# Optimization experiments

Measured on AMD Instinct MI355X. Metric: run time of the kernel, lower is better.

Reference implementation:

```python
import jax, jax.numpy as jnp
import numpy as np

B, T, D, U = 4096, 50, 128, 128  # batch, history len, embed dim, GRU units (U==D)
ATT_H1, ATT_H2 = 128, 64         # Attention MLP hiddens (hard-coded in source)
DH1, DH2 = 256, 128              # deep model hiddens
BN_EPS = 1e-3
LEAKY = 0.0003


def setup_inputs() -> dict:
    key = jax.random.key(0)
    ks = iter(jax.random.split(key, 40))
    n = lambda shape, s=0.05: jax.random.normal(next(ks), shape, dtype=jnp.float32) * s
    DI = U + D  # deep_input dim
    return {
        "inputs": n((B, T + 1, D), 1.0),
        # Keras GRU (reset_after=True): kernel, recurrent kernel, bias[2,3U] (input/recurrent)
        "gru_W": n((D, 3 * U)), "gru_U": n((U, 3 * U)), "gru_b": n((2, 3 * U)),
        # Attention MLP: input is concat([h, news-h, news, h*news]) -> 4U
        "att_W1": n((4 * U, ATT_H1)), "att_b1": n((ATT_H1,)),
        "att_W2": n((ATT_H1, ATT_H2)), "att_b2": n((ATT_H2,)),
        "att_W3": n((ATT_H2, 1)), "att_b3": n((1,)),
        # AUGRU Bilinear gates: Dense(U, bias) on inputs, Dense(U, no bias) on state
        "au_Wu": n((U, U)), "au_bu": n((U,)), "au_Uu": n((U, U)),
        "au_Wr": n((U, U)), "au_br": n((U,)), "au_Ur": n((U, U)),
        "au_Wc": n((U, U)), "au_bc": n((U,)), "au_Uc": n((U, U)),
        # deep model: BN (inference) + 2 leaky-relu Dense + sigmoid head
        "bn_gamma": jnp.ones((DI,), jnp.float32), "bn_beta": jnp.zeros((DI,), jnp.float32),
        "bn_mean": jnp.zeros((DI,), jnp.float32), "bn_var": jnp.ones((DI,), jnp.float32),
        "d_W1": n((DI, DH1)), "d_b1": n((DH1,)),
        "d_W2": n((DH1, DH2)), "d_b2": n((DH2,)),
        "f_W": n((DH2, 1)), "f_b": n((1,)),
    }


def _gru(x_seq, W, Ur, b):
    # Keras GRU, reset_after=True, gate order [z, r, h]
    Xp = jnp.einsum('btd,dk->btk', x_seq, W) + b[0]  # precompute input projections
    h0 = jnp.zeros((x_seq.shape[0], Ur.shape[0]), x_seq.dtype)

    def step(h, xp):
        hp = h @ Ur + b[1]
        xz, xr, xh = jnp.split(xp, 3, axis=-1)
        hz, hr, hh = jnp.split(hp, 3, axis=-1)
        z = jax.nn.sigmoid(xz + hz)
        r = jax.nn.sigmoid(xr + hr)
        hc = jnp.tanh(xh + r * hh)
        hn = z * h + (1.0 - z) * hc
        return hn, hn

    _, hs = jax.lax.scan(step, h0, jnp.swapaxes(Xp, 0, 1))
    return jnp.swapaxes(hs, 0, 1)  # [B,T,U]


def reference(inputs, gru_W, gru_U, gru_b,
              att_W1, att_b1, att_W2, att_b2, att_W3, att_b3,
              au_Wu, au_bu, au_Uu, au_Wr, au_br, au_Ur, au_Wc, au_bc, au_Uc,
              bn_gamma, bn_beta, bn_mean, bn_var,
              d_W1, d_b1, d_W2, d_b2, f_W, f_b):
    hist = inputs[:, :-1, :]   # [B,T,D]
    news = inputs[:, -1, :]    # [B,D]

    hs = _gru(hist, gru_W, gru_U, gru_b)  # [B,T,U]

    # Attention (vectorized over the per-timestep Python loop; same math)
    news_b = jnp.broadcast_to(news[:, None, :], hs.shape)
    emb = jnp.concatenate([hs, news_b - hs, news_b, hs * news_b], axis=-1)  # [B,T,4U]
    a = jax.nn.relu(jnp.einsum('bti,ij->btj', emb, att_W1) + att_b1)
    a = jax.nn.relu(jnp.einsum('bti,ij->btj', a, att_W2) + att_b2)
    ats = jax.nn.sigmoid(jnp.einsum('bti,ij->btj', a, att_W3) + att_b3)  # [B,T,1]

    # AUGRU: precompute input-side projections, scan the recurrence
    xu = jnp.einsum('btd,dk->btk', hs, au_Wu) + au_bu
    xr = jnp.einsum('btd,dk->btk', hs, au_Wr) + au_br
    xc = jnp.einsum('btd,dk->btk', hs, au_Wc) + au_bc

    def au_step(h, xs):
        xu_t, xr_t, xc_t, at_t = xs
        u = jax.nn.sigmoid(xu_t + h @ au_Uu)
        r = jax.nn.sigmoid(xr_t + h @ au_Ur)
        c = jnp.tanh(xc_t + r * (h @ au_Uc))
        u_ = at_t * u
        hn = (1.0 - u_) * h + u_ * c
        return hn, None

    h0 = jnp.zeros_like(hs[:, 0, :])
    xs = (jnp.swapaxes(xu, 0, 1), jnp.swapaxes(xr, 0, 1),
          jnp.swapaxes(xc, 0, 1), jnp.swapaxes(ats, 0, 1))
    h_final, _ = jax.lax.scan(au_step, h0, xs)

    # deep model: BN (inference) -> Dense + leaky ReLU x2 -> sigmoid head
    x = jnp.concatenate([h_final, news], axis=-1)
    x = (x - bn_mean) * jax.lax.rsqrt(bn_var + BN_EPS) * bn_gamma + bn_beta
    x = x @ d_W1 + d_b1
    x = jnp.where(x >= 0, x, LEAKY * x)
    x = x @ d_W2 + d_b2
    x = jnp.where(x >= 0, x, LEAKY * x)
    y = jax.nn.sigmoid(x @ f_W + f_b)  # [B,1]
    return y
```

## Files before the change

kernel.cpp:

```cpp
#include <hip/hip_runtime.h>
#include <hip/hip_bf16.h>
#include <math.h>


#define LK 0.0003f

typedef __attribute__((ext_vector_type(8))) short short8;
typedef __attribute__((ext_vector_type(4))) float f32x4;

union U8 { short8 s; unsigned short u[8]; };

__device__ __forceinline__ float sigf(float x) {
    return __builtin_amdgcn_rcpf(1.0f + __expf(-x));
}
__device__ __forceinline__ float tanhfast(float x) {
    return fmaf(2.0f, __builtin_amdgcn_rcpf(1.0f + __expf(-2.0f * x)), -1.0f);
}
__device__ __forceinline__ float lky(float v) { return v >= 0.0f ? v : LK * v; }
__device__ __forceinline__ unsigned short f2bf(float f) {
    __bf16 b = (__bf16)f;
    return *reinterpret_cast<unsigned short*>(&b);
}
__device__ __forceinline__ unsigned pk2(float a, float b) {
    return (unsigned)f2bf(a) | ((unsigned)f2bf(b) << 16);
}
__device__ __forceinline__ float bf2f(unsigned short h) {
    return __uint_as_float(((unsigned)h) << 16);
}
__device__ __forceinline__ int swz(int row, int kbyte, int stride) {
    return row * stride + (kbyte ^ ((row & 7) << 4));
}
__device__ __forceinline__ f32x4 mfma16(short8 a, short8 b, f32x4 c) {
    return __builtin_amdgcn_mfma_f32_16x16x32_bf16(a, b, c, 0, 0, 0);
}
__device__ __forceinline__ void barrier_lds() {
    __builtin_amdgcn_sched_barrier(0);
    asm volatile("s_waitcnt lgkmcnt(0)" ::: "memory");
    __builtin_amdgcn_sched_barrier(0);
    __builtin_amdgcn_s_barrier();
    __builtin_amdgcn_sched_barrier(0);
}

__global__ void pack_all(
    const float* __restrict__ gW, const float* __restrict__ gU,
    const float* __restrict__ aWu, const float* __restrict__ aWr, const float* __restrict__ aWc,
    const float* __restrict__ aUu, const float* __restrict__ aUr, const float* __restrict__ aUc,
    const float* __restrict__ tW1, const float* __restrict__ tW2,
    const float* __restrict__ dW1, const float* __restrict__ dW2,
    const float* __restrict__ abu, const float* __restrict__ abr, const float* __restrict__ abc,
    unsigned short* __restrict__ Wg, unsigned short* __restrict__ Ug,
    unsigned short* __restrict__ Wau, unsigned short* __restrict__ Uau,
    unsigned short* __restrict__ WA, unsigned short* __restrict__ WN,
    unsigned short* __restrict__ AW2,
    unsigned short* __restrict__ DW1, unsigned short* __restrict__ DW2,
    float* __restrict__ bp)
{
    int i = blockIdx.x * 256 + threadIdx.x;
    if (i < 49152) {
        int n = i >> 7, k = i & 127;
        Wg[i] = f2bf(gW[k * 384 + n]);
        Ug[i] = f2bf(gU[k * 384 + n]);
    } else if (i < 98304) {
        int j = i - 49152; int n = j >> 7, k = j & 127;
        int g = n >> 7, c = n & 127;
        const float* s = (g == 0) ? aWu : (g == 1) ? aWr : aWc;
        const float* u = (g == 0) ? aUu : (g == 1) ? aUr : aUc;
        Wau[j] = f2bf(s[k * 128 + c]);
        Uau[j] = f2bf(u[k * 128 + c]);
    } else if (i < 131072) {
        int j = i - 98304; int n = j >> 8, k = j & 255;
        float v = (k < 128) ? (tW1[k * 128 + n] - tW1[(128 + k) * 128 + n])
                            : tW1[(384 + (k - 128)) * 128 + n];
        WA[j] = f2bf(v);
    } else if (i < 147456) {
        int j = i - 131072; int n = j >> 7, k = j & 127;
        WN[j] = f2bf(tW1[(128 + k) * 128 + n] + tW1[(256 + k) * 128 + n]);
    } else if (i < 155648) {
        int j = i - 147456; int n = j >> 7, k = j & 127;
        AW2[j] = f2bf(tW2[k * 64 + n]);
    } else if (i < 221184) {
        int j = i - 155648; int n = j >> 8, k = j & 255;
        DW1[j] = f2bf(dW1[k * 256 + n]);
    } else if (i < 253952) {
        int j = i - 221184; int n = j >> 8, k = j & 255;
        DW2[j] = f2bf(dW2[k * 128 + n]);
    } else if (i < 254336) {
        int j = i - 253952;
        bp[j] = (j < 128) ? abu[j] : (j < 256) ? abr[j - 128] : abc[j - 256];
    }
}

__global__ __launch_bounds__(512, 2) void nterm_kernel(
    const float* __restrict__ inputs, const unsigned short* __restrict__ WN,
    const float* __restrict__ b1, float* __restrict__ nterm)
{
    __shared__ __align__(16) unsigned char nb[64 * 256];

    const int tid = threadIdx.x;
    const int wv = tid >> 6, l = tid & 63, l15 = l & 15, lg = l >> 4;
    const size_t b0 = (size_t)blockIdx.x * 64;

    {
        int r = tid >> 3, c = tid & 7;
        const float* src = inputs + ((b0 + r) * 51 + 50) * 128 + c * 16;
        float4 v0 = *(const float4*)(src);
        float4 v1 = *(const float4*)(src + 4);
        float4 v2 = *(const float4*)(src + 8);
        float4 v3 = *(const float4*)(src + 12);
        *(uint4*)(nb + swz(r, c * 32, 256)) =
            make_uint4(pk2(v0.x, v0.y), pk2(v0.z, v0.w), pk2(v1.x, v1.y), pk2(v1.z, v1.w));
        *(uint4*)(nb + swz(r, c * 32 + 16, 256)) =
            make_uint4(pk2(v2.x, v2.y), pk2(v2.z, v2.w), pk2(v3.x, v3.y), pk2(v3.z, v3.w));
    }
    __syncthreads();

    short8 wf[4];
#pragma unroll
    for (int kt = 0; kt < 4; ++kt)
        wf[kt] = *(const short8*)(WN + (wv * 16 + l15) * 128 + kt * 32 + lg * 8);

    f32x4 acc[4];
#pragma unroll
    for (int rt = 0; rt < 4; ++rt) acc[rt] = (f32x4){0.f, 0.f, 0.f, 0.f};
#pragma unroll
    for (int rt = 0; rt < 4; ++rt)
#pragma unroll
        for (int kt = 0; kt < 4; ++kt) {
            short8 axx = *(const short8*)(nb + swz(rt * 16 + l15, kt * 64 + lg * 16, 256));
            acc[rt] = mfma16(axx, wf[kt], acc[rt]);
        }
    float bb = b1[wv * 16 + l15];
#pragma unroll
    for (int rt = 0; rt < 4; ++rt)
#pragma unroll
        for (int j = 0; j < 4; ++j)
            nterm[(b0 + rt * 16 + lg * 4 + j) * 128 + wv * 16 + l15] = acc[rt][j] + bb;
}

__global__ __launch_bounds__(512, 2) void gru_attn(
    const float* __restrict__ inputs, const unsigned short* __restrict__ Wt,
    const unsigned short* __restrict__ Ut, const float* __restrict__ gb,
    const unsigned short* __restrict__ WA, const unsigned short* __restrict__ AW2,
    const float* __restrict__ ab2, const float* __restrict__ nterm,
    const float* __restrict__ W3, const float* __restrict__ b3,
    uint2* __restrict__ hs4, float* __restrict__ ats)
{
    __shared__ __align__(16) unsigned char xbuf[2][4096];
    __shared__ __align__(16) unsigned char hbuf[2][4096];
    __shared__ __align__(16) unsigned char pbuf[2][4096];
    __shared__ __align__(16) unsigned char a1buf[2][4096];
    __shared__ float a2buf[2][16 * 65];
    __shared__ float w3l[64];

    const int tid = threadIdx.x;
    const int wv = tid >> 6, l = tid & 63, l15 = l & 15, lg = l >> 4;
    const size_t row0 = (size_t)blockIdx.x * 16;
    const int ucol = wv * 16 + l15;

    short8 wf[3][4], uf[3][4];
#pragma unroll
    for (int g = 0; g < 3; ++g)
#pragma unroll
        for (int kt = 0; kt < 4; ++kt) {
            int n = g * 128 + ucol;
            int k0 = kt * 32 + lg * 8;
            wf[g][kt] = *(const short8*)(Wt + n * 128 + k0);
            uf[g][kt] = *(const short8*)(Ut + n * 128 + k0);
        }
    short8 waf[8];
#pragma unroll
    for (int kt = 0; kt < 8; ++kt)
        waf[kt] = *(const short8*)(WA + ucol * 256 + kt * 32 + lg * 8);
    short8 w2f[4];
    const int n2 = (wv & 3) * 16 + l15;
    if (wv < 4) {
#pragma unroll
        for (int kt = 0; kt < 4; ++kt)
            w2f[kt] = *(const short8*)(AW2 + n2 * 128 + kt * 32 + lg * 8);
    }
    const float b2v = (wv < 4) ? ab2[n2] : 0.f;
    const float b3v = b3[0];
    if (tid < 64) w3l[tid] = W3[tid];

    const float bx2 = gb[256 + ucol], bh2 = gb[640 + ucol];
    const float bz  = gb[ucol] + gb[384 + ucol];
    const float br  = gb[128 + ucol] + gb[512 + ucol];

    float nt4[4], news4[4];
#pragma unroll
    for (int j = 0; j < 4; ++j) {
        int m = lg * 4 + j;
        nt4[j]   = nterm[(row0 + m) * 128 + ucol];
        news4[j] = inputs[((row0 + m) * 51 + 50) * 128 + ucol];
    }
    uint2* hs4p = hs4 + ((row0 >> 2) + lg) * 6400 + ucol;

    const int sr = tid >> 5, ss = tid & 31;
    const float* xsrc = inputs + (row0 + sr) * 51 * 128 + ss * 4;

    int rdo[4], wro[4];
#pragma unroll
    for (int kt = 0; kt < 4; ++kt) rdo[kt] = swz(l15, kt * 64 + lg * 16, 256);
#pragma unroll
    for (int j = 0; j < 4; ++j)   wro[j] = swz(lg * 4 + j, ucol * 2, 256);
    const int xwo = swz(sr, ss * 8, 256);

    *(uint2*)(hbuf[0] + tid * 8) = make_uint2(0u, 0u);
    {
        float4 v = *(const float4*)(xsrc);
        *(uint2*)(xbuf[0] + xwo) = make_uint2(pk2(v.x, v.y), pk2(v.z, v.w));
    }
    float hreg[4] = {0.f, 0.f, 0.f, 0.f};
    __syncthreads();

#define STEP(T, PF, DOGRU, DOL1, DOL2, DODOT) do {                                  \
    const int p_ = (T) & 1;                                                          \
    float4 xpf_;                                                                     \
    if (PF) xpf_ = *(const float4*)(xsrc + (size_t)((T) + 1) * 128);                 \
    short8 ah_[4];                                                                   \
    if (DOGRU || DOL1) {                                                             \
        _Pragma("unroll")                                                            \
        for (int kt = 0; kt < 4; ++kt)                                               \
            ah_[kt] = *(const short8*)(hbuf[p_] + rdo[kt]);                          \
    }                                                                                \
    short8 ax_[4], pa_[4];                                                           \
    if (DOGRU) {                                                                     \
        _Pragma("unroll")                                                            \
        for (int kt = 0; kt < 4; ++kt)                                               \
            ax_[kt] = *(const short8*)(xbuf[p_] + rdo[kt]);                          \
    }                                                                                \
    if (DOL1) {                                                                      \
        _Pragma("unroll")                                                            \
        for (int kt = 0; kt < 4; ++kt)                                               \
            pa_[kt] = *(const short8*)(pbuf[p_] + rdo[kt]);                          \
    }                                                                                \
    f32x4 accx_[3], acch_[3], lacc_;                                                 \
    __builtin_amdgcn_s_setprio(1);                                                   \
    if (DOGRU) {                                                                     \
        _Pragma("unroll")                                                            \
        for (int g = 0; g < 3; ++g) {                                                \
            accx_[g] = (f32x4){0.f, 0.f, 0.f, 0.f};                                  \
            acch_[g] = (f32x4){0.f, 0.f, 0.f, 0.f};                                  \
        }                                                                            \
        _Pragma("unroll")                                                            \
        for (int kt = 0; kt < 4; ++kt)                                               \
            _Pragma("unroll")                                                        \
            for (int g = 0; g < 3; ++g) {                                            \
                accx_[g] = mfma16(ax_[kt], wf[g][kt], accx_[g]);                     \
                acch_[g] = mfma16(ah_[kt], uf[g][kt], acch_[g]);                     \
            }                                                                        \
    }                                                                                \
    if (DOL1) {                                                                      \
        lacc_ = (f32x4){0.f, 0.f, 0.f, 0.f};                                         \
        _Pragma("unroll")                                                            \
        for (int kt = 0; kt < 4; ++kt) lacc_ = mfma16(ah_[kt], waf[kt], lacc_);      \
        _Pragma("unroll")                                                            \
        for (int kt = 0; kt < 4; ++kt) lacc_ = mfma16(pa_[kt], waf[4 + kt], lacc_);  \
    }                                                                                \
    __builtin_amdgcn_s_setprio(0);                                                   \
    if (DOGRU) {                                                                     \
        unsigned short hbv_[4];                                                      \
        _Pragma("unroll")                                                            \
        for (int j = 0; j < 4; ++j) {                                                \
            float z  = sigf(accx_[0][j] + acch_[0][j] + bz);                         \
            float r  = sigf(accx_[1][j] + acch_[1][j] + br);                         \
            float hc = tanhfast(accx_[2][j] + bx2 + r * (acch_[2][j] + bh2));        \
            float hn = fmaf(z, hreg[j] - hc, hc);                                    \
            hreg[j] = hn;                                                            \
            hbv_[j] = f2bf(hn);                                                      \
            *(unsigned short*)(hbuf[p_ ^ 1] + wro[j]) = hbv_[j];                     \
            *(unsigned short*)(pbuf[p_ ^ 1] + wro[j]) = f2bf(hn * news4[j]);         \
        }                                                                            \
        hs4p[(size_t)(T) * 128] =                                                    \
            make_uint2((unsigned)hbv_[0] | ((unsigned)hbv_[1] << 16),                \
                       (unsigned)hbv_[2] | ((unsigned)hbv_[3] << 16));               \
    }                                                                                \
    if (DOL1) {                                                                      \
        _Pragma("unroll")                                                            \
        for (int j = 0; j < 4; ++j) {                                                \
            float v = fmaxf(lacc_[j] + nt4[j], 0.f);                                 \
            *(unsigned short*)(a1buf[p_] + wro[j]) = f2bf(v);                        \
        }                                                                            \
    }                                                                                \
    if (DOL2) {                                                                      \
        if (wv < 4) {                                                                \
            f32x4 c2_ = (f32x4){0.f, 0.f, 0.f, 0.f};                                 \
            _Pragma("unroll")                                                        \
            for (int kt = 0; kt < 4; ++kt) {                                         \
                short8 aa_ = *(const short8*)(a1buf[p_ ^ 1] + rdo[kt]);              \
                c2_ = mfma16(aa_, w2f[kt], c2_);                                     \
            }                                                                        \
            _Pragma("unroll")                                                        \
            for (int j = 0; j < 4; ++j)                                              \
                a2buf[p_][(lg * 4 + j) * 65 + n2] = fmaxf(c2_[j] + b2v, 0.f);        \
        }                                                                            \
    }                                                                                \
    if (DODOT) {                                                                     \
        if (tid >= 256) {                         \
            int rrow_ = (tid - 256) >> 4, cc_ = tid & 15;                            \
            const float* a2r_ = &a2buf[p_ ^ 1][rrow_ * 65];                          \
            float s_ = a2r_[cc_] * w3l[cc_] + a2r_[cc_ + 16] * w3l[cc_ + 16]         \
                     + a2r_[cc_ + 32] * w3l[cc_ + 32] + a2r_[cc_ + 48] * w3l[cc_ + 48];\
            s_ += __shfl_xor(s_, 8, 16);                                             \
            s_ += __shfl_xor(s_, 4, 16);                                             \
            s_ += __shfl_xor(s_, 2, 16);                                             \
            s_ += __shfl_xor(s_, 1, 16);                                             \
            if ((tid & 15) == 0)                                                     \
                ats[(row0 + rrow_) * 50 + ((T) - 3)] = sigf(s_ + b3v);               \
        }                                                                            \
    }                                                                                \
    if (PF)                                                                          \
        *(uint2*)(xbuf[p_ ^ 1] + xwo) =                                              \
            make_uint2(pk2(xpf_.x, xpf_.y), pk2(xpf_.z, xpf_.w));                    \
    barrier_lds();                                                                   \
} while (0)

    STEP(0, 1, 1, 0, 0, 0);
    STEP(1, 1, 1, 1, 0, 0);
    STEP(2, 1, 1, 1, 1, 0);
    for (int t = 3; t <= 48; ++t) STEP(t, 1, 1, 1, 1, 1);
    STEP(49, 0, 1, 1, 1, 1);
    STEP(50, 0, 0, 1, 1, 1);
    STEP(51, 0, 0, 0, 1, 1);
    STEP(52, 0, 0, 0, 0, 1);
#undef STEP
}

__global__ __launch_bounds__(512, 2) void augru_mfma(
    const uint2* __restrict__ hs4, const unsigned short* __restrict__ Wt,
    const unsigned short* __restrict__ Ut, const float* __restrict__ bp,
    const float* __restrict__ ats, float* __restrict__ hf)
{
    __shared__ __align__(16) unsigned char xbuf[2][4096];
    __shared__ __align__(16) unsigned char hbuf[2][4096];
    __shared__ float atsl[16 * 50];

    const int tid = threadIdx.x;
    const int wv = tid >> 6, l = tid & 63, l15 = l & 15, lg = l >> 4;
    const size_t row0 = (size_t)blockIdx.x * 16;
    const int ucol = wv * 16 + l15;

    short8 wf[3][4], uf[3][4];
#pragma unroll
    for (int g = 0; g < 3; ++g)
#pragma unroll
        for (int kt = 0; kt < 4; ++kt) {
            int n = g * 128 + ucol;
            int k0 = kt * 32 + lg * 8;
            wf[g][kt] = *(const short8*)(Wt + n * 128 + k0);
            uf[g][kt] = *(const short8*)(Ut + n * 128 + k0);
        }
    const float bx0 = bp[ucol], bx1 = bp[128 + ucol], bx2 = bp[256 + ucol];

    const int sg = tid >> 7, sc = tid & 127;
    const uint2* xsrc2 = hs4 + ((row0 >> 2) + sg) * 6400 + sc;

    int rdo[4], wro[4];
#pragma unroll
    for (int kt = 0; kt < 4; ++kt) rdo[kt] = swz(l15, kt * 64 + lg * 16, 256);
#pragma unroll
    for (int j = 0; j < 4; ++j)   wro[j] = swz(lg * 4 + j, ucol * 2, 256);
    int xwo4[4];
#pragma unroll
    for (int q = 0; q < 4; ++q)   xwo4[q] = swz(4 * sg + q, sc * 2, 256);

    *(uint2*)(hbuf[0] + tid * 8) = make_uint2(0u, 0u);
    if (tid < 400) {
        atsl[tid] = ats[row0 * 50 + tid];
        atsl[tid + 400] = ats[row0 * 50 + tid + 400];
    }
    {
        uint2 u = xsrc2[0];
        *(unsigned short*)(xbuf[0] + xwo4[0]) = (unsigned short)(u.x & 0xffff);
        *(unsigned short*)(xbuf[0] + xwo4[1]) = (unsigned short)(u.x >> 16);
        *(unsigned short*)(xbuf[0] + xwo4[2]) = (unsigned short)(u.y & 0xffff);
        *(unsigned short*)(xbuf[0] + xwo4[3]) = (unsigned short)(u.y >> 16);
    }
    float hreg[4] = {0.f, 0.f, 0.f, 0.f};
    __syncthreads();

    for (int t = 0; t < 50; ++t) {
        const int p = t & 1;
        uint2 xnext;
        if (t < 49) xnext = xsrc2[(size_t)(t + 1) * 128];

        short8 ax[4], ah[4];
#pragma unroll
        for (int kt = 0; kt < 4; ++kt) {
            ax[kt] = *(const short8*)(xbuf[p] + rdo[kt]);
            ah[kt] = *(const short8*)(hbuf[p] + rdo[kt]);
        }
        f32x4 accx[3], acch[3];
#pragma unroll
        for (int g = 0; g < 3; ++g) {
            accx[g] = (f32x4){0.f, 0.f, 0.f, 0.f};
            acch[g] = (f32x4){0.f, 0.f, 0.f, 0.f};
        }
        __builtin_amdgcn_s_setprio(1);
#pragma unroll
        for (int kt = 0; kt < 4; ++kt)
#pragma unroll
            for (int g = 0; g < 3; ++g) {
                accx[g] = mfma16(ax[kt], wf[g][kt], accx[g]);
                acch[g] = mfma16(ah[kt], uf[g][kt], acch[g]);
            }
        __builtin_amdgcn_s_setprio(0);
#pragma unroll
        for (int j = 0; j < 4; ++j) {
            int m = lg * 4 + j;
            float u  = sigf(accx[0][j] + bx0 + acch[0][j]);
            float r  = sigf(accx[1][j] + bx1 + acch[1][j]);
            float c  = tanhfast(accx[2][j] + bx2 + r * acch[2][j]);
            float uu = atsl[m * 50 + t] * u;
            float hn = fmaf(uu, c - hreg[j], hreg[j]);
            hreg[j] = hn;
            *(unsigned short*)(hbuf[p ^ 1] + wro[j]) = f2bf(hn);
        }
        if (t < 49) {
            *(unsigned short*)(xbuf[p ^ 1] + xwo4[0]) = (unsigned short)(xnext.x & 0xffff);
            *(unsigned short*)(xbuf[p ^ 1] + xwo4[1]) = (unsigned short)(xnext.x >> 16);
            *(unsigned short*)(xbuf[p ^ 1] + xwo4[2]) = (unsigned short)(xnext.y & 0xffff);
            *(unsigned short*)(xbuf[p ^ 1] + xwo4[3]) = (unsigned short)(xnext.y >> 16);
        }
        barrier_lds();
    }
#pragma unroll
    for (int j = 0; j < 4; ++j)
        hf[(row0 + lg * 4 + j) * 128 + ucol] = hreg[j];
}

__global__ __launch_bounds__(256, 2) void final_mfma(
    const float* __restrict__ hfv, const float* __restrict__ inputs,
    const float* __restrict__ gam, const float* __restrict__ bet,
    const float* __restrict__ mu, const float* __restrict__ var,
    const unsigned short* __restrict__ W1t, const float* __restrict__ b1,
    const unsigned short* __restrict__ W2t, const float* __restrict__ b2,
    const float* __restrict__ fW, const float* __restrict__ fb,
    float* __restrict__ out)
{
    __shared__ __align__(16) unsigned char xnb[16 * 512];
    __shared__ __align__(16) unsigned char d1b[16 * 512];
    __shared__ float d2b[16 * 132];
    __shared__ float wfl[128];

    const int tid = threadIdx.x;
    const int wv = tid >> 6, l = tid & 63, l15 = l & 15, lg = l >> 4;
    const size_t r0 = (size_t)blockIdx.x * 16;

    short8 w1f[4][8];
#pragma unroll
    for (int p = 0; p < 4; ++p)
#pragma unroll
        for (int kt = 0; kt < 8; ++kt) {
            int n = wv * 64 + p * 16 + l15;
            w1f[p][kt] = *(const short8*)(W1t + n * 256 + kt * 32 + lg * 8);
        }
    short8 w2f[2][8];
#pragma unroll
    for (int p = 0; p < 2; ++p)
#pragma unroll
        for (int kt = 0; kt < 8; ++kt) {
            int n = wv * 32 + p * 16 + l15;
            w2f[p][kt] = *(const short8*)(W2t + n * 256 + kt * 32 + lg * 8);
        }
    if (tid < 128) wfl[tid] = fW[tid];

    {
        int r = tid >> 4, c = tid & 15, k0 = c * 16;
        float v[16];
#pragma unroll
        for (int q = 0; q < 16; ++q) {
            int k = k0 + q;
            float x = (k < 128) ? hfv[(r0 + r) * 128 + k]
                                : inputs[((r0 + r) * 51 + 50) * 128 + (k - 128)];
            float s = gam[k] * rsqrtf(var[k] + 0.001f);
            v[q] = (x - mu[k]) * s + bet[k];
        }
        *(uint4*)(xnb + swz(r, k0 * 2, 512)) =
            make_uint4(pk2(v[0], v[1]), pk2(v[2], v[3]), pk2(v[4], v[5]), pk2(v[6], v[7]));
        *(uint4*)(xnb + swz(r, k0 * 2 + 16, 512)) =
            make_uint4(pk2(v[8], v[9]), pk2(v[10], v[11]), pk2(v[12], v[13]), pk2(v[14], v[15]));
    }
    __syncthreads();

    f32x4 a1[4];
#pragma unroll
    for (int p = 0; p < 4; ++p) a1[p] = (f32x4){0.f, 0.f, 0.f, 0.f};
#pragma unroll
    for (int kt = 0; kt < 8; ++kt) {
        short8 axx = *(const short8*)(xnb + swz(l15, kt * 64 + lg * 16, 512));
#pragma unroll
        for (int p = 0; p < 4; ++p) a1[p] = mfma16(axx, w1f[p][kt], a1[p]);
    }
#pragma unroll
    for (int p = 0; p < 4; ++p) {
        float bb = b1[wv * 64 + p * 16 + l15];
#pragma unroll
        for (int j = 0; j < 4; ++j) {
            int row = lg * 4 + j, col = wv * 64 + p * 16 + l15;
            *(unsigned short*)(d1b + swz(row, col * 2, 512)) = f2bf(lky(a1[p][j] + bb));
        }
    }
    __syncthreads();

    f32x4 a2[2];
#pragma unroll
    for (int p = 0; p < 2; ++p) a2[p] = (f32x4){0.f, 0.f, 0.f, 0.f};
#pragma unroll
    for (int kt = 0; kt < 8; ++kt) {
        short8 axx = *(const short8*)(d1b + swz(l15, kt * 64 + lg * 16, 512));
#pragma unroll
        for (int p = 0; p < 2; ++p) a2[p] = mfma16(axx, w2f[p][kt], a2[p]);
    }
#pragma unroll
    for (int p = 0; p < 2; ++p) {
        float bb = b2[wv * 32 + p * 16 + l15];
#pragma unroll
        for (int j = 0; j < 4; ++j)
            d2b[(lg * 4 + j) * 132 + wv * 32 + p * 16 + l15] = lky(a2[p][j] + bb);
    }
    __syncthreads();

    if (tid < 16) {
        float s = fb[0];
#pragma unroll 8
        for (int k = 0; k < 128; ++k) s += d2b[tid * 132 + k] * wfl[k];
        out[r0 + tid] = sigf(s);
    }
}

extern "C" void kernel_launch(void* const* d_in, const int* in_sizes, int n_in,
                              void* d_out, int out_size, void* d_ws, size_t ws_size,
                              hipStream_t stream)
{
    const float* inputs   = (const float*)d_in[0];
    const float* gru_W    = (const float*)d_in[1];
    const float* gru_U    = (const float*)d_in[2];
    const float* gru_b    = (const float*)d_in[3];
    const float* att_W1   = (const float*)d_in[4];
    const float* att_b1   = (const float*)d_in[5];
    const float* att_W2   = (const float*)d_in[6];
    const float* att_b2   = (const float*)d_in[7];
    const float* att_W3   = (const float*)d_in[8];
    const float* att_b3   = (const float*)d_in[9];
    const float* au_Wu    = (const float*)d_in[10];
    const float* au_bu    = (const float*)d_in[11];
    const float* au_Uu    = (const float*)d_in[12];
    const float* au_Wr    = (const float*)d_in[13];
    const float* au_br    = (const float*)d_in[14];
    const float* au_Ur    = (const float*)d_in[15];
    const float* au_Wc    = (const float*)d_in[16];
    const float* au_bc    = (const float*)d_in[17];
    const float* au_Uc    = (const float*)d_in[18];
    const float* bn_gamma = (const float*)d_in[19];
    const float* bn_beta  = (const float*)d_in[20];
    const float* bn_mean  = (const float*)d_in[21];
    const float* bn_var   = (const float*)d_in[22];
    const float* d_W1     = (const float*)d_in[23];
    const float* d_b1     = (const float*)d_in[24];
    const float* d_W2     = (const float*)d_in[25];
    const float* d_b2     = (const float*)d_in[26];
    const float* f_W      = (const float*)d_in[27];
    const float* f_b      = (const float*)d_in[28];

    char* w = (char*)d_ws;
    uint2* hs4          = (uint2*)w;
    float* ats          = (float*)(w + 52428800);
    float* hf           = (float*)(w + 53248000);
    float* nterm        = (float*)(w + 55345152);
    unsigned short* Wg  = (unsigned short*)(w + 57442304);
    unsigned short* Ug  = (unsigned short*)(w + 57540608);
    unsigned short* Wau = (unsigned short*)(w + 57638912);
    unsigned short* Uau = (unsigned short*)(w + 57737216);
    unsigned short* WA  = (unsigned short*)(w + 57835520);
    unsigned short* WN  = (unsigned short*)(w + 57901056);
    unsigned short* AW2 = (unsigned short*)(w + 57933824);
    unsigned short* DW1 = (unsigned short*)(w + 57950208);
    unsigned short* DW2 = (unsigned short*)(w + 58081280);
    float* bp           = (float*)(w + 58146816);

    pack_all<<<994, 256, 0, stream>>>(
        gru_W, gru_U, au_Wu, au_Wr, au_Wc, au_Uu, au_Ur, au_Uc,
        att_W1, att_W2, d_W1, d_W2, au_bu, au_br, au_bc,
        Wg, Ug, Wau, Uau, WA, WN, AW2, DW1, DW2, bp);
    nterm_kernel<<<64, 512, 0, stream>>>(inputs, WN, att_b1, nterm);
    gru_attn<<<256, 512, 0, stream>>>(inputs, Wg, Ug, gru_b, WA, AW2, att_b2,
                                      nterm, att_W3, att_b3, hs4, ats);
    augru_mfma<<<256, 512, 0, stream>>>(hs4, Wau, Uau, bp, ats, hf);
    final_mfma<<<256, 256, 0, stream>>>(hf, inputs, bn_gamma, bn_beta, bn_mean, bn_var,
                                        DW1, d_b1, DW2, d_b2, f_W, f_b, (float*)d_out);
}
```

Baseline: 167.1 us.

## Fuse AUGRU recurrence into GRU+attention kernel via wavefront-skewed pipeline

Merges the GRU/attention kernel and the AUGRU kernel into one. The AUGRU step runs four timesteps behind the GRU step inside the same loop, reading GRU states from a 5-slot LDS ring and attention scores from LDS. This removes the global round trip of the hidden-state sequence and attention weights, plus one kernel launch. To free registers for the extra AUGRU weight fragments, the attention W1/W2 weights move from registers into swizzled LDS. The cost is more LDS traffic, higher register pressure and longer per-step critical paths, which may hurt occupancy.

```diff
diff --git a/kernel.cpp b/kernel.cpp
--- a/kernel.cpp
+++ b/kernel.cpp
@@ -7,8 +7,6 @@
 
 typedef __attribute__((ext_vector_type(8))) short short8;
 typedef __attribute__((ext_vector_type(4))) float f32x4;
-
-union U8 { short8 s; unsigned short u[8]; };
 
 __device__ __forceinline__ float sigf(float x) {
     return __builtin_amdgcn_rcpf(1.0f + __expf(-x));
@@ -23,9 +21,6 @@
 }
 __device__ __forceinline__ unsigned pk2(float a, float b) {
     return (unsigned)f2bf(a) | ((unsigned)f2bf(b) << 16);
-}
-__device__ __forceinline__ float bf2f(unsigned short h) {
-    return __uint_as_float(((unsigned)h) << 16);
 }
 __device__ __forceinline__ int swz(int row, int kbyte, int stride) {
     return row * stride + (kbyte ^ ((row & 7) << 4));
@@ -137,19 +132,24 @@
             nterm[(b0 + rt * 16 + lg * 4 + j) * 128 + wv * 16 + l15] = acc[rt][j] + bb;
 }
 
-__global__ __launch_bounds__(512, 2) void gru_attn(
+__global__ __launch_bounds__(512, 2) void dien_rec(
     const float* __restrict__ inputs, const unsigned short* __restrict__ Wt,
     const unsigned short* __restrict__ Ut, const float* __restrict__ gb,
     const unsigned short* __restrict__ WA, const unsigned short* __restrict__ AW2,
     const float* __restrict__ ab2, const float* __restrict__ nterm,
     const float* __restrict__ W3, const float* __restrict__ b3,
-    uint2* __restrict__ hs4, float* __restrict__ ats)
+    const unsigned short* __restrict__ Wau, const unsigned short* __restrict__ Uau,
+    const float* __restrict__ bp, float* __restrict__ hf)
 {
+    __shared__ __align__(16) unsigned char WAl[128 * 512];
+    __shared__ __align__(16) unsigned char AW2l[64 * 256];
     __shared__ __align__(16) unsigned char xbuf[2][4096];
-    __shared__ __align__(16) unsigned char hbuf[2][4096];
+    __shared__ __align__(16) unsigned char hring[5][4096];
     __shared__ __align__(16) unsigned char pbuf[2][4096];
     __shared__ __align__(16) unsigned char a1buf[2][4096];
+    __shared__ __align__(16) unsigned char h2buf[2][4096];
     __shared__ float a2buf[2][16 * 65];
+    __shared__ float atsl[16 * 50];
     __shared__ float w3l[64];
 
     const int tid = threadIdx.x;
@@ -157,27 +157,29 @@
     const size_t row0 = (size_t)blockIdx.x * 16;
     const int ucol = wv * 16 + l15;
 
-    short8 wf[3][4], uf[3][4];
+    short8 wf[3][4], uf[3][4], wau[3][4], uau[3][4];
 #pragma unroll
     for (int g = 0; g < 3; ++g)
 #pragma unroll
         for (int kt = 0; kt < 4; ++kt) {
             int n = g * 128 + ucol;
             int k0 = kt * 32 + lg * 8;
-            wf[g][kt] = *(const short8*)(Wt + n * 128 + k0);
-            uf[g][kt] = *(const short8*)(Ut + n * 128 + k0);
+            wf[g][kt]  = *(const short8*)(Wt  + n * 128 + k0);
+            uf[g][kt]  = *(const short8*)(Ut  + n * 128 + k0);
+            wau[g][kt] = *(const short8*)(Wau + n * 128 + k0);
+            uau[g][kt] = *(const short8*)(Uau + n * 128 + k0);
         }
-    short8 waf[8];
-#pragma unroll
-    for (int kt = 0; kt < 8; ++kt)
-        waf[kt] = *(const short8*)(WA + ucol * 256 + kt * 32 + lg * 8);
-    short8 w2f[4];
+    for (int i = tid; i < 4096; i += 512) {
+        int n = i >> 5, kk = (i & 31) * 8;
+        *(short8*)(WAl + n * 512 + ((kk * 2) ^ ((n & 7) << 4))) =
+            *(const short8*)(WA + n * 256 + kk);
+    }
+    for (int i = tid; i < 1024; i += 512) {
+        int n = i >> 4, kk = (i & 15) * 8;
+        *(short8*)(AW2l + n * 256 + ((kk * 2) ^ ((n & 7) << 4))) =
+            *(const short8*)(AW2 + n * 128 + kk);
+    }
     const int n2 = (wv & 3) * 16 + l15;
-    if (wv < 4) {
-#pragma unroll
-        for (int kt = 0; kt < 4; ++kt)
-            w2f[kt] = *(const short8*)(AW2 + n2 * 128 + kt * 32 + lg * 8);
-    }
     const float b2v = (wv < 4) ? ab2[n2] : 0.f;
     const float b3v = b3[0];
     if (tid < 64) w3l[tid] = W3[tid];
@@ -185,6 +187,7 @@
     const float bx2 = gb[256 + ucol], bh2 = gb[640 + ucol];
     const float bz  = gb[ucol] + gb[384 + ucol];
     const float br  = gb[128 + ucol] + gb[512 + ucol];
+    const float ba0 = bp[ucol], ba1 = bp[128 + ucol], ba2 = bp[256 + ucol];
 
     float nt4[4], news4[4];
 #pragma unroll
@@ -193,55 +196,59 @@
         nt4[j]   = nterm[(row0 + m) * 128 + ucol];
         news4[j] = inputs[((row0 + m) * 51 + 50) * 128 + ucol];
     }
-    uint2* hs4p = hs4 + ((row0 >> 2) + lg) * 6400 + ucol;
 
     const int sr = tid >> 5, ss = tid & 31;
     const float* xsrc = inputs + (row0 + sr) * 51 * 128 + ss * 4;
 
-    int rdo[4], wro[4];
+    int rdo[4], wro[4], wafo[8], w2o[4];
 #pragma unroll
     for (int kt = 0; kt < 4; ++kt) rdo[kt] = swz(l15, kt * 64 + lg * 16, 256);
 #pragma unroll
     for (int j = 0; j < 4; ++j)   wro[j] = swz(lg * 4 + j, ucol * 2, 256);
+#pragma unroll
+    for (int kt = 0; kt < 8; ++kt)
+        wafo[kt] = ucol * 512 + ((kt * 64 + lg * 16) ^ ((ucol & 7) << 4));
+#pragma unroll
+    for (int kt = 0; kt < 4; ++kt)
+        w2o[kt] = n2 * 256 + ((kt * 64 + lg * 16) ^ ((n2 & 7) << 4));
     const int xwo = swz(sr, ss * 8, 256);
 
-    *(uint2*)(hbuf[0] + tid * 8) = make_uint2(0u, 0u);
+    *(uint2*)(hring[4] + tid * 8) = make_uint2(0u, 0u);
+    *(uint2*)(h2buf[0] + tid * 8) = make_uint2(0u, 0u);
     {
         float4 v = *(const float4*)(xsrc);
         *(uint2*)(xbuf[0] + xwo) = make_uint2(pk2(v.x, v.y), pk2(v.z, v.w));
     }
-    float hreg[4] = {0.f, 0.f, 0.f, 0.f};
+    float hreg[4]  = {0.f, 0.f, 0.f, 0.f};
+    float h2reg[4] = {0.f, 0.f, 0.f, 0.f};
     __syncthreads();
 
-#define STEP(T, PF, DOGRU, DOL1, DOL2, DODOT) do {                                  \
+#define STEP(T, PF, DOGRU, DOL1, DOL2, DODOT, DOAU) do {                            \
     const int p_ = (T) & 1;                                                          \
+    const int rdslot_ = ((T) + 4) % 5;                                  \
+    const int wrslot_ = (T) % 5;                                            \
+    const int x2slot_ = ((T) + 1) % 5;                                  \
     float4 xpf_;                                                                     \
     if (PF) xpf_ = *(const float4*)(xsrc + (size_t)((T) + 1) * 128);                 \
     short8 ah_[4];                                                                   \
     if (DOGRU || DOL1) {                                                             \
         _Pragma("unroll")                                                            \
         for (int kt = 0; kt < 4; ++kt)                                               \
-            ah_[kt] = *(const short8*)(hbuf[p_] + rdo[kt]);                          \
+            ah_[kt] = *(const short8*)(hring[rdslot_] + rdo[kt]);                    \
     }                                                                                \
-    short8 ax_[4], pa_[4];                                                           \
+                                                           \
     if (DOGRU) {                                                                     \
+        short8 ax_[4];                                                               \
         _Pragma("unroll")                                                            \
         for (int kt = 0; kt < 4; ++kt)                                               \
             ax_[kt] = *(const short8*)(xbuf[p_] + rdo[kt]);                          \
-    }                                                                                \
-    if (DOL1) {                                                                      \
-        _Pragma("unroll")                                                            \
-        for (int kt = 0; kt < 4; ++kt)                                               \
-            pa_[kt] = *(const short8*)(pbuf[p_] + rdo[kt]);                          \
-    }                                                                                \
-    f32x4 accx_[3], acch_[3], lacc_;                                                 \
-    __builtin_amdgcn_s_setprio(1);                                                   \
-    if (DOGRU) {                                                                     \
+        f32x4 accx_[3], acch_[3];                                                    \
         _Pragma("unroll")                                                            \
         for (int g = 0; g < 3; ++g) {                                                \
             accx_[g] = (f32x4){0.f, 0.f, 0.f, 0.f};                                  \
             acch_[g] = (f32x4){0.f, 0.f, 0.f, 0.f};                                  \
         }                                                                            \
+        __builtin_amdgcn_s_setprio(1);                                               \
         _Pragma("unroll")                                                            \
         for (int kt = 0; kt < 4; ++kt)                                               \
             _Pragma("unroll")                                                        \
@@ -249,17 +256,7 @@
                 accx_[g] = mfma16(ax_[kt], wf[g][kt], accx_[g]);                     \
                 acch_[g] = mfma16(ah_[kt], uf[g][kt], acch_[g]);                     \
             }                                                                        \
-    }                                                                                \
-    if (DOL1) {                                                                      \
-        lacc_ = (f32x4){0.f, 0.f, 0.f, 0.f};                                         \
-        _Pragma("unroll")                                                            \
-        for (int kt = 0; kt < 4; ++kt) lacc_ = mfma16(ah_[kt], waf[kt], lacc_);      \
-        _Pragma("unroll")                                                            \
-        for (int kt = 0; kt < 4; ++kt) lacc_ = mfma16(pa_[kt], waf[4 + kt], lacc_);  \
-    }                                                                                \
-    __builtin_amdgcn_s_setprio(0);                                                   \
-    if (DOGRU) {                                                                     \
-        unsigned short hbv_[4];                                                      \
+        __builtin_amdgcn_s_setprio(0);                                               \
         _Pragma("unroll")                                                            \
         for (int j = 0; j < 4; ++j) {                                                \
             float z  = sigf(accx_[0][j] + acch_[0][j] + bz);                         \
@@ -267,36 +264,50 @@
             float hc = tanhfast(accx_[2][j] + bx2 + r * (acch_[2][j] + bh2));        \
             float hn = fmaf(z, hreg[j] - hc, hc);                                    \
             hreg[j] = hn;                                                            \
-            hbv_[j] = f2bf(hn);                                                      \
-            *(unsigned short*)(hbuf[p_ ^ 1] + wro[j]) = hbv_[j];                     \
+            *(unsigned short*)(hring[wrslot_] + wro[j]) = f2bf(hn);                  \
             *(unsigned short*)(pbuf[p_ ^ 1] + wro[j]) = f2bf(hn * news4[j]);         \
         }                                                                            \
-        hs4p[(size_t)(T) * 128] =                                                    \
-            make_uint2((unsigned)hbv_[0] | ((unsigned)hbv_[1] << 16),                \
-                       (unsigned)hbv_[2] | ((unsigned)hbv_[3] << 16));               \
     }                                                                                \
+                                                      \
     if (DOL1) {                                                                      \
+        f32x4 lacc_ = (f32x4){0.f, 0.f, 0.f, 0.f};                                   \
+        __builtin_amdgcn_s_setprio(1);                                               \
+        _Pragma("unroll")                                                            \
+        for (int kt = 0; kt < 4; ++kt) {                                             \
+            short8 wa_ = *(const short8*)(WAl + wafo[kt]);                           \
+            lacc_ = mfma16(ah_[kt], wa_, lacc_);                                     \
+        }                                                                            \
+        _Pragma("unroll")                                                            \
+        for (int kt = 0; kt < 4; ++kt) {                                             \
+            short8 pa_ = *(const short8*)(pbuf[p_] + rdo[kt]);                       \
+            short8 wa_ = *(const short8*)(WAl + wafo[4 + kt]);                       \
+            lacc_ = mfma16(pa_, wa_, lacc_);                                         \
+        }                                                                            \
+        __builtin_amdgcn_s_setprio(0);                                               \
         _Pragma("unroll")                                                            \
         for (int j = 0; j < 4; ++j) {                                                \
             float v = fmaxf(lacc_[j] + nt4[j], 0.f);                                 \
             *(unsigned short*)(a1buf[p_] + wro[j]) = f2bf(v);                        \
         }                                                                            \
     }                                                                                \
+                                          \
     if (DOL2) {                                                                      \
         if (wv < 4) {                                                                \
             f32x4 c2_ = (f32x4){0.f, 0.f, 0.f, 0.f};                                 \
             _Pragma("unroll")                                                        \
             for (int kt = 0; kt < 4; ++kt) {                                         \
                 short8 aa_ = *(const short8*)(a1buf[p_ ^ 1] + rdo[kt]);              \
-                c2_ = mfma16(aa_, w2f[kt], c2_);                                     \
+                short8 w2_ = *(const short8*)(AW2l + w2o[kt]);                       \
+                c2_ = mfma16(aa_, w2_, c2_);                                         \
             }                                                                        \
             _Pragma("unroll")                                                        \
             for (int j = 0; j < 4; ++j)                                              \
                 a2buf[p_][(lg * 4 + j) * 65 + n2] = fmaxf(c2_[j] + b2v, 0.f);        \
         }                                                                            \
     }                                                                                \
+                                              \
     if (DODOT) {                                                                     \
-        if (tid >= 256) {                         \
+        if (tid >= 256) {                                                            \
             int rrow_ = (tid - 256) >> 4, cc_ = tid & 15;                            \
             const float* a2r_ = &a2buf[p_ ^ 1][rrow_ * 65];                          \
             float s_ = a2r_[cc_] * w3l[cc_] + a2r_[cc_ + 16] * w3l[cc_ + 16]         \
@@ -305,8 +316,43 @@
             s_ += __shfl_xor(s_, 4, 16);                                             \
             s_ += __shfl_xor(s_, 2, 16);                                             \
             s_ += __shfl_xor(s_, 1, 16);                                             \
-            if ((tid & 15) == 0)                                                     \
-                ats[(row0 + rrow_) * 50 + ((T) - 3)] = sigf(s_ + b3v);               \
+            if ((tid & 15) == 0) atsl[rrow_ * 50 + ((T) - 3)] = sigf(s_ + b3v);      \
+        }                                                                            \
+    }                                                                                \
+                                                   \
+    if (DOAU) {                                                                      \
+        const int pa2_ = ((T) - 4) & 1;                                              \
+        short8 x2_[4], h2_[4];                                                       \
+        _Pragma("unroll")                                                            \
+        for (int kt = 0; kt < 4; ++kt) {                                             \
+            x2_[kt] = *(const short8*)(hring[x2slot_] + rdo[kt]);                    \
+            h2_[kt] = *(const short8*)(h2buf[pa2_] + rdo[kt]);                       \
+        }                                                                            \
+        f32x4 au_x_[3], au_h_[3];                                                    \
+        _Pragma("unroll")                                                            \
+        for (int g = 0; g < 3; ++g) {                                                \
+            au_x_[g] = (f32x4){0.f, 0.f, 0.f, 0.f};                                  \
+            au_h_[g] = (f32x4){0.f, 0.f, 0.f, 0.f};                                  \
+        }                                                                            \
+        __builtin_amdgcn_s_setprio(1);                                               \
+        _Pragma("unroll")                                                            \
+        for (int kt = 0; kt < 4; ++kt)                                               \
+            _Pragma("unroll")                                                        \
+            for (int g = 0; g < 3; ++g) {                                            \
+                au_x_[g] = mfma16(x2_[kt], wau[g][kt], au_x_[g]);                    \
+                au_h_[g] = mfma16(h2_[kt], uau[g][kt], au_h_[g]);                    \
+            }                                                                        \
+        __builtin_amdgcn_s_setprio(0);                                               \
+        _Pragma("unroll")                                                            \
+        for (int j = 0; j < 4; ++j) {                                                \
+            int m = lg * 4 + j;                                                      \
+            float u  = sigf(au_x_[0][j] + ba0 + au_h_[0][j]);                        \
+            float r  = sigf(au_x_[1][j] + ba1 + au_h_[1][j]);                        \
+            float c  = tanhfast(au_x_[2][j] + ba2 + r * au_h_[2][j]);                \
+            float uu = atsl[m * 50 + ((T) - 4)] * u;                                 \
+            float hn = fmaf(uu, c - h2reg[j], h2reg[j]);                             \
+            h2reg[j] = hn;                                                           \
+            *(unsigned short*)(h2buf[pa2_ ^ 1] + wro[j]) = f2bf(hn);                 \
         }                                                                            \
     }                                                                                \
     if (PF)                                                                          \
@@ -315,118 +361,21 @@
     barrier_lds();                                                                   \
 } while (0)
 
-    STEP(0, 1, 1, 0, 0, 0);
-    STEP(1, 1, 1, 1, 0, 0);
-    STEP(2, 1, 1, 1, 1, 0);
-    for (int t = 3; t <= 48; ++t) STEP(t, 1, 1, 1, 1, 1);
-    STEP(49, 0, 1, 1, 1, 1);
-    STEP(50, 0, 0, 1, 1, 1);
-    STEP(51, 0, 0, 0, 1, 1);
-    STEP(52, 0, 0, 0, 0, 1);
+    STEP(0, 1, 1, 0, 0, 0, 0);
+    STEP(1, 1, 1, 1, 0, 0, 0);
+    STEP(2, 1, 1, 1, 1, 0, 0);
+    STEP(3, 1, 1, 1, 1, 1, 0);
+    for (int t = 4; t <= 48; ++t) STEP(t, 1, 1, 1, 1, 1, 1);
+    STEP(49, 0, 1, 1, 1, 1, 1);
+    STEP(50, 0, 0, 1, 1, 1, 1);
+    STEP(51, 0, 0, 0, 1, 1, 1);
+    STEP(52, 0, 0, 0, 0, 1, 1);
+    STEP(53, 0, 0, 0, 0, 0, 1);
 #undef STEP
-}
-
-__global__ __launch_bounds__(512, 2) void augru_mfma(
-    const uint2* __restrict__ hs4, const unsigned short* __restrict__ Wt,
-    const unsigned short* __restrict__ Ut, const float* __restrict__ bp,
-    const float* __restrict__ ats, float* __restrict__ hf)
-{
-    __shared__ __align__(16) unsigned char xbuf[2][4096];
-    __shared__ __align__(16) unsigned char hbuf[2][4096];
-    __shared__ float atsl[16 * 50];
-
-    const int tid = threadIdx.x;
-    const int wv = tid >> 6, l = tid & 63, l15 = l & 15, lg = l >> 4;
-    const size_t row0 = (size_t)blockIdx.x * 16;
-    const int ucol = wv * 16 + l15;
-
-    short8 wf[3][4], uf[3][4];
-#pragma unroll
-    for (int g = 0; g < 3; ++g)
-#pragma unroll
-        for (int kt = 0; kt < 4; ++kt) {
-            int n = g * 128 + ucol;
-            int k0 = kt * 32 + lg * 8;
-            wf[g][kt] = *(const short8*)(Wt + n * 128 + k0);
-            uf[g][kt] = *(const short8*)(Ut + n * 128 + k0);
-        }
-    const float bx0 = bp[ucol], bx1 = bp[128 + ucol], bx2 = bp[256 + ucol];
-
-    const int sg = tid >> 7, sc = tid & 127;
-    const uint2* xsrc2 = hs4 + ((row0 >> 2) + sg) * 6400 + sc;
-
-    int rdo[4], wro[4];
-#pragma unroll
-    for (int kt = 0; kt < 4; ++kt) rdo[kt] = swz(l15, kt * 64 + lg * 16, 256);
-#pragma unroll
-    for (int j = 0; j < 4; ++j)   wro[j] = swz(lg * 4 + j, ucol * 2, 256);
-    int xwo4[4];
-#pragma unroll
-    for (int q = 0; q < 4; ++q)   xwo4[q] = swz(4 * sg + q, sc * 2, 256);
-
-    *(uint2*)(hbuf[0] + tid * 8) = make_uint2(0u, 0u);
-    if (tid < 400) {
-        atsl[tid] = ats[row0 * 50 + tid];
-        atsl[tid + 400] = ats[row0 * 50 + tid + 400];
-    }
-    {
-        uint2 u = xsrc2[0];
-        *(unsigned short*)(xbuf[0] + xwo4[0]) = (unsigned short)(u.x & 0xffff);
-        *(unsigned short*)(xbuf[0] + xwo4[1]) = (unsigned short)(u.x >> 16);
-        *(unsigned short*)(xbuf[0] + xwo4[2]) = (unsigned short)(u.y & 0xffff);
-        *(unsigned short*)(xbuf[0] + xwo4[3]) = (unsigned short)(u.y >> 16);
-    }
-    float hreg[4] = {0.f, 0.f, 0.f, 0.f};
-    __syncthreads();
-
-    for (int t = 0; t < 50; ++t) {
-        const int p = t & 1;
-        uint2 xnext;
-        if (t < 49) xnext = xsrc2[(size_t)(t + 1) * 128];
-
-        short8 ax[4], ah[4];
-#pragma unroll
-        for (int kt = 0; kt < 4; ++kt) {
-            ax[kt] = *(const short8*)(xbuf[p] + rdo[kt]);
-            ah[kt] = *(const short8*)(hbuf[p] + rdo[kt]);
-        }
-        f32x4 accx[3], acch[3];
-#pragma unroll
-        for (int g = 0; g < 3; ++g) {
-            accx[g] = (f32x4){0.f, 0.f, 0.f, 0.f};
-            acch[g] = (f32x4){0.f, 0.f, 0.f, 0.f};
-        }
-        __builtin_amdgcn_s_setprio(1);
-#pragma unroll
-        for (int kt = 0; kt < 4; ++kt)
-#pragma unroll
-            for (int g = 0; g < 3; ++g) {
-                accx[g] = mfma16(ax[kt], wf[g][kt], accx[g]);
-                acch[g] = mfma16(ah[kt], uf[g][kt], acch[g]);
-            }
-        __builtin_amdgcn_s_setprio(0);
-#pragma unroll
-        for (int j = 0; j < 4; ++j) {
-            int m = lg * 4 + j;
-            float u  = sigf(accx[0][j] + bx0 + acch[0][j]);
-            float r  = sigf(accx[1][j] + bx1 + acch[1][j]);
-            float c  = tanhfast(accx[2][j] + bx2 + r * acch[2][j]);
-            float uu = atsl[m * 50 + t] * u;
-            float hn = fmaf(uu, c - hreg[j], hreg[j]);
-            hreg[j] = hn;
-            *(unsigned short*)(hbuf[p ^ 1] + wro[j]) = f2bf(hn);
-        }
-        if (t < 49) {
-            *(unsigned short*)(xbuf[p ^ 1] + xwo4[0]) = (unsigned short)(xnext.x & 0xffff);
-            *(unsigned short*)(xbuf[p ^ 1] + xwo4[1]) = (unsigned short)(xnext.x >> 16);
-            *(unsigned short*)(xbuf[p ^ 1] + xwo4[2]) = (unsigned short)(xnext.y & 0xffff);
-            *(unsigned short*)(xbuf[p ^ 1] + xwo4[3]) = (unsigned short)(xnext.y >> 16);
-        }
-        barrier_lds();
-    }
+
 #pragma unroll
     for (int j = 0; j < 4; ++j)
-        hf[(row0 + lg * 4 + j) * 128 + ucol] = hreg[j];
+        hf[(row0 + lg * 4 + j) * 128 + ucol] = h2reg[j];
 }
 
 __global__ __launch_bounds__(256, 2) void final_mfma(
@@ -564,8 +513,6 @@
     const float* f_b      = (const float*)d_in[28];
 
     char* w = (char*)d_ws;
-    uint2* hs4          = (uint2*)w;
-    float* ats          = (float*)(w + 52428800);
     float* hf           = (float*)(w + 53248000);
     float* nterm        = (float*)(w + 55345152);
     unsigned short* Wg  = (unsigned short*)(w + 57442304);
@@ -584,9 +531,8 @@
         att_W1, att_W2, d_W1, d_W2, au_bu, au_br, au_bc,
         Wg, Ug, Wau, Uau, WA, WN, AW2, DW1, DW2, bp);
     nterm_kernel<<<64, 512, 0, stream>>>(inputs, WN, att_b1, nterm);
-    gru_attn<<<256, 512, 0, stream>>>(inputs, Wg, Ug, gru_b, WA, AW2, att_b2,
-                                      nterm, att_W3, att_b3, hs4, ats);
-    augru_mfma<<<256, 512, 0, stream>>>(hs4, Wau, Uau, bp, ats, hf);
+    dien_rec<<<256, 512, 0, stream>>>(inputs, Wg, Ug, gru_b, WA, AW2, att_b2,
+                                      nterm, att_W3, att_b3, Wau, Uau, bp, hf);
     final_mfma<<<256, 256, 0, stream>>>(hf, inputs, bn_gamma, bn_beta, bn_mean, bn_var,
                                         DW1, d_b1, DW2, d_b2, f_W, f_b, (float*)d_out);
 }
```

After: 367.1 us. 120% more time.
